# Kernel tuning notes

Measured on AMD Instinct MI355X. Metric: run time of the kernel, lower is better.

## Reference

```python
import jax, jax.numpy as jnp
import numpy as np

VOCAB, EMB, HID, L = 100000, 128, 256, 9
B, S = 128, 512
H = HID // 2  # per-direction hidden size
PAD = 0


def setup_inputs() -> dict:
    key = jax.random.key(0)
    ks = jax.random.split(key, 18)
    seqs = jax.random.randint(ks[0], (B, S), 1, VOCAB)
    # left-aligned padding: lengths in [S//2, S]
    lens = jax.random.randint(ks[1], (B,), S // 2, S + 1)
    seqs = jnp.where(jnp.arange(S)[None, :] < lens[:, None], seqs, PAD)
    labels = jax.random.randint(ks[2], (B, S), 0, L)

    def n(k, shape, s=0.05):
        return jax.random.normal(k, shape, jnp.float32) * s

    emb = n(ks[3], (VOCAB, EMB)).at[PAD].set(0.0)
    inp = {
        'sequences': seqs, 'labels': labels, 'emb': emb,
        'w_ih_f': n(ks[4], (4 * H, EMB)), 'w_hh_f': n(ks[5], (4 * H, H)),
        'b_ih_f': n(ks[6], (4 * H,)), 'b_hh_f': n(ks[7], (4 * H,)),
        'w_ih_b': n(ks[8], (4 * H, EMB)), 'w_hh_b': n(ks[9], (4 * H, H)),
        'b_ih_b': n(ks[10], (4 * H,)), 'b_hh_b': n(ks[11], (4 * H,)),
        'w_out': n(ks[12], (L, HID)), 'b_out': n(ks[13], (L,)),
        'start_t': n(ks[14], (L,), 0.1), 'end_t': n(ks[15], (L,), 0.1),
        'trans': n(ks[16], (L, L), 0.1),
    }
    return inp


def _lstm_scan(x, w_ih, w_hh, b_ih, b_hh):
    # x: [S, B, E] -> hidden states [S, B, H]
    h0 = jnp.zeros((x.shape[1], w_hh.shape[1]), x.dtype)

    def step(carry, xt):
        h, c = carry
        g = xt @ w_ih.T + b_ih + h @ w_hh.T + b_hh
        i, f, gg, o = jnp.split(g, 4, axis=-1)  # PyTorch gate order i,f,g,o
        c = jax.nn.sigmoid(f) * c + jax.nn.sigmoid(i) * jnp.tanh(gg)
        h = jax.nn.sigmoid(o) * jnp.tanh(c)
        return (h, c), h

    _, hs = jax.lax.scan(step, (h0, h0), x)
    return hs


def reference(sequences, labels, emb, w_ih_f, w_hh_f, b_ih_f, b_hh_f,
              w_ih_b, w_hh_b, b_ih_b, b_hh_b, w_out, b_out,
              start_t, end_t, trans):
    # Embedding lookup (dropout is identity at inference)
    x = emb[sequences]                      # [B,S,E]
    xt = jnp.swapaxes(x, 0, 1)              # [S,B,E]
    hf = _lstm_scan(xt, w_ih_f, w_hh_f, b_ih_f, b_hh_f)
    hb = _lstm_scan(xt[::-1], w_ih_b, w_hh_b, b_ih_b, b_hh_b)[::-1]
    hcat = jnp.concatenate([hf, hb], axis=-1)         # [S,B,HID]
    emissions = jnp.swapaxes(hcat, 0, 1) @ w_out.T + b_out  # [B,S,L]

    mask = sequences != PAD                 # [B,S], first step all True
    maskf = mask.astype(emissions.dtype)

    # --- CRF numerator (score of gold path) ---
    em_tag = jnp.take_along_axis(emissions, labels[..., None], axis=2)[..., 0]  # [B,S]
    trans_sc = trans[labels[:, :-1], labels[:, 1:]]                              # [B,S-1]
    num = start_t[labels[:, 0]] + em_tag[:, 0] \
        + jnp.sum((trans_sc + em_tag[:, 1:]) * maskf[:, 1:], axis=1)
    seq_ends = jnp.sum(mask, axis=1) - 1
    last_tags = labels[jnp.arange(labels.shape[0]), seq_ends]
    num = num + end_t[last_tags]

    # --- CRF partition function (forward algorithm) ---
    def fstep(score, inp):
        em_t, m_t = inp  # [B,L], [B]
        nxt = jax.nn.logsumexp(score[:, :, None] + trans[None] + em_t[:, None, :], axis=1)
        return jnp.where(m_t[:, None], nxt, score), None

    score0 = start_t[None, :] + emissions[:, 0]  # [B,L]
    em_rest = jnp.swapaxes(emissions, 0, 1)[1:]  # [S-1,B,L]
    scoreT, _ = jax.lax.scan(fstep, score0, (em_rest, mask.T[1:]))
    denom = jax.nn.logsumexp(scoreT + end_t[None, :], axis=1)  # [B]

    # model returns -log_likelihood (torchcrf default reduction='sum')
    return -jnp.sum(num - denom)
```

## Files before the change

### kernel.cpp

```cpp
#include <hip/hip_runtime.h>
#include <hip/hip_bf16.h>

#define B_   128
#define S_   512
#define H_   128
#define G_   512
#define EMB_ 128
#define NL_  9

typedef __attribute__((ext_vector_type(8))) short bf16x8;
typedef __attribute__((ext_vector_type(4))) short bf16x4;
typedef __attribute__((ext_vector_type(4))) float f32x4;
typedef unsigned short ushort_t;

__device__ __forceinline__ void wg_bar() {
    asm volatile("s_waitcnt lgkmcnt(0)\n\ts_barrier" ::: "memory");
}

__device__ __forceinline__ float bfbits2f(short s) {
    unsigned int u = ((unsigned int)(unsigned short)s) << 16;
    return __builtin_bit_cast(float, u);
}
__device__ __forceinline__ short f2bf(float f) {
    unsigned int u = __builtin_bit_cast(unsigned int, f);
    u += 0x7FFFu + ((u >> 16) & 1u);
    return (short)(u >> 16);
}
__device__ __forceinline__ unsigned int pack2(float lo, float hi) {
    return (unsigned int)(unsigned short)f2bf(lo) | ((unsigned int)(unsigned short)f2bf(hi) << 16);
}
__device__ __forceinline__ float exp2_(float x) {
    float r; asm("v_exp_f32 %0, %1" : "=v"(r) : "v"(x)); return r;
}
__device__ __forceinline__ float log2_(float x) {
    float r; asm("v_log_f32 %0, %1" : "=v"(r) : "v"(x)); return r;
}
__device__ __forceinline__ float max3_(float a, float b, float c) {
    float r; asm("v_max3_f32 %0, %1, %2, %3" : "=v"(r) : "v"(a), "v"(b), "v"(c)); return r;
}
__device__ __forceinline__ float tanh_(float x) {
    return 1.f - 2.f * __builtin_amdgcn_rcpf(1.f + exp2_(2.8853900817779268f * x));
}
__device__ __forceinline__ bf16x8 cvt8(float4 a, float4 b) {
    bf16x8 r;
    r[0] = f2bf(a.x); r[1] = f2bf(a.y); r[2] = f2bf(a.z); r[3] = f2bf(a.w);
    r[4] = f2bf(b.x); r[5] = f2bf(b.y); r[6] = f2bf(b.z); r[7] = f2bf(b.w);
    return r;
}

#define MINIGEMM(tl, bufsel)                                                       \
    {                                                                              \
      f32x4 x0 = {biasI[tl][0], biasI[tl][0], biasI[tl][0], biasI[tl][0]};         \
      f32x4 x1 = {biasI[tl][1], biasI[tl][1], biasI[tl][1], biasI[tl][1]};         \
      f32x4 x2 = {biasI[tl][2], biasI[tl][2], biasI[tl][2], biasI[tl][2]};         \
      f32x4 x3 = {biasI[tl][3], biasI[tl][3], biasI[tl][3], biasI[tl][3]};         \
      x0 = __builtin_amdgcn_mfma_f32_16x16x32_bf16(afE0, bfragI[tl][0][0], x0, 0, 0, 0); \
      x1 = __builtin_amdgcn_mfma_f32_16x16x32_bf16(afE0, bfragI[tl][1][0], x1, 0, 0, 0); \
      x2 = __builtin_amdgcn_mfma_f32_16x16x32_bf16(afE0, bfragI[tl][2][0], x2, 0, 0, 0); \
      x3 = __builtin_amdgcn_mfma_f32_16x16x32_bf16(afE0, bfragI[tl][3][0], x3, 0, 0, 0); \
      x0 = __builtin_amdgcn_mfma_f32_16x16x32_bf16(afE1, bfragI[tl][0][1], x0, 0, 0, 0); \
      x1 = __builtin_amdgcn_mfma_f32_16x16x32_bf16(afE1, bfragI[tl][1][1], x1, 0, 0, 0); \
      x2 = __builtin_amdgcn_mfma_f32_16x16x32_bf16(afE1, bfragI[tl][2][1], x2, 0, 0, 0); \
      x3 = __builtin_amdgcn_mfma_f32_16x16x32_bf16(afE1, bfragI[tl][3][1], x3, 0, 0, 0); \
      x0 = __builtin_amdgcn_mfma_f32_16x16x32_bf16(afE2, bfragI[tl][0][2], x0, 0, 0, 0); \
      x1 = __builtin_amdgcn_mfma_f32_16x16x32_bf16(afE2, bfragI[tl][1][2], x1, 0, 0, 0); \
      x2 = __builtin_amdgcn_mfma_f32_16x16x32_bf16(afE2, bfragI[tl][2][2], x2, 0, 0, 0); \
      x3 = __builtin_amdgcn_mfma_f32_16x16x32_bf16(afE2, bfragI[tl][3][2], x3, 0, 0, 0); \
      x0 = __builtin_amdgcn_mfma_f32_16x16x32_bf16(afE3, bfragI[tl][0][3], x0, 0, 0, 0); \
      x1 = __builtin_amdgcn_mfma_f32_16x16x32_bf16(afE3, bfragI[tl][1][3], x1, 0, 0, 0); \
      x2 = __builtin_amdgcn_mfma_f32_16x16x32_bf16(afE3, bfragI[tl][2][3], x2, 0, 0, 0); \
      x3 = __builtin_amdgcn_mfma_f32_16x16x32_bf16(afE3, bfragI[tl][3][3], x3, 0, 0, 0); \
      short* dstp = xwSW + (bufsel) * 8192 + (wv * 32 + (tl) * 16 + n16) * 4;      \
      _Pragma("unroll")                                                            \
      for (int r = 0; r < 4; r++) {                                                \
        uint2 wq; wq.x = pack2(x0[r], x1[r]); wq.y = pack2(x2[r], x3[r]);          \
        *(uint2*)(dstp + (quad * 4 + r) * 512) = wq;                               \
      }                                                                            \
    }

#define STEPK(k)                                                                   \
  {                                                                                \
    if ((k) == 0 && s4 == 0 && m < 31) {                                           \
      int t0s = dir ? (S_ - 32 - m16) : (m16 + 16);                                \
      int tok = seq[b * S_ + t0s + n16];                                           \
      const float* ep = emb + (size_t)tok * EMB_ + quad * 8;                       \
      e0 = *(const float4*)(ep);        e1 = *(const float4*)(ep + 4);             \
      e2 = *(const float4*)(ep + 32);   e3 = *(const float4*)(ep + 36);            \
      e4 = *(const float4*)(ep + 64);   e5 = *(const float4*)(ep + 68);            \
      e6 = *(const float4*)(ep + 96);   e7 = *(const float4*)(ep + 100);           \
    }                                                                              \
    bf16x8 af0 = hbuf[(k) & 1][0 * 4 + quad];                                      \
    bf16x8 af1 = hbuf[(k) & 1][1 * 4 + quad];                                      \
    bf16x8 af2 = hbuf[(k) & 1][2 * 4 + quad];                                      \
    bf16x8 af3 = hbuf[(k) & 1][3 * 4 + quad];                                      \
    const int KE = s4x4 + (k);                                                     \
    const int slot = dir ? (15 - KE) : KE;                                         \
    bf16x4 xvg = *(const bf16x4*)(xwS + (m & 1) * 8192 + slot * 512 + uu * 4);     \
    if ((k) == 0 && s4 == 1 && m < 31) { afE0 = cvt8(e0, e1); afE1 = cvt8(e2, e3); } \
    if ((k) == 2 && s4 == 1 && m < 31) { afE2 = cvt8(e4, e5); afE3 = cvt8(e6, e7); } \
    if ((k) == 0 && s4 == 2 && m < 31) MINIGEMM(0, ((m & 1) ^ 1))                  \
    if ((k) == 2 && s4 == 2 && m < 31) MINIGEMM(1, ((m & 1) ^ 1))                  \
    if ((k) == 1 && s4 == 0 && m >= 1 && wv == 3 && lane < 36) {                   \
      int a0 = dir ? (S_ - m16) : (m16 - 16);                                      \
      float4 fv = *(const float4*)(emL + (a0 & 31) * 9 + lane * 4);                \
      *(float4*)(emdir + (size_t)b * (S_ * NL_) + a0 * NL_ + lane * 4) = fv;       \
    }                                                                              \
    f32x4 aA0 = __builtin_amdgcn_mfma_f32_16x16x32_bf16(af0, bfrag[0][0][0], ZACC, 0, 0, 0); \
    f32x4 aA1 = __builtin_amdgcn_mfma_f32_16x16x32_bf16(af0, bfrag[0][1][0], ZACC, 0, 0, 0); \
    f32x4 aA2 = __builtin_amdgcn_mfma_f32_16x16x32_bf16(af0, bfrag[0][2][0], ZACC, 0, 0, 0); \
    f32x4 aA3 = __builtin_amdgcn_mfma_f32_16x16x32_bf16(af0, bfrag[0][3][0], ZACC, 0, 0, 0); \
    f32x4 aB0 = __builtin_amdgcn_mfma_f32_16x16x32_bf16(af0, bfrag[1][0][0], ZACC, 0, 0, 0); \
    f32x4 aB1 = __builtin_amdgcn_mfma_f32_16x16x32_bf16(af0, bfrag[1][1][0], ZACC, 0, 0, 0); \
    f32x4 aB2 = __builtin_amdgcn_mfma_f32_16x16x32_bf16(af0, bfrag[1][2][0], ZACC, 0, 0, 0); \
    f32x4 aB3 = __builtin_amdgcn_mfma_f32_16x16x32_bf16(af0, bfrag[1][3][0], ZACC, 0, 0, 0); \
    aA0 = __builtin_amdgcn_mfma_f32_16x16x32_bf16(af1, bfrag[0][0][1], aA0, 0, 0, 0); \
    aA1 = __builtin_amdgcn_mfma_f32_16x16x32_bf16(af1, bfrag[0][1][1], aA1, 0, 0, 0); \
    aA2 = __builtin_amdgcn_mfma_f32_16x16x32_bf16(af1, bfrag[0][2][1], aA2, 0, 0, 0); \
    aA3 = __builtin_amdgcn_mfma_f32_16x16x32_bf16(af1, bfrag[0][3][1], aA3, 0, 0, 0); \
    aB0 = __builtin_amdgcn_mfma_f32_16x16x32_bf16(af1, bfrag[1][0][1], aB0, 0, 0, 0); \
    aB1 = __builtin_amdgcn_mfma_f32_16x16x32_bf16(af1, bfrag[1][1][1], aB1, 0, 0, 0); \
    aB2 = __builtin_amdgcn_mfma_f32_16x16x32_bf16(af1, bfrag[1][2][1], aB2, 0, 0, 0); \
    aB3 = __builtin_amdgcn_mfma_f32_16x16x32_bf16(af1, bfrag[1][3][1], aB3, 0, 0, 0); \
    aA0 = __builtin_amdgcn_mfma_f32_16x16x32_bf16(af2, bfrag[0][0][2], aA0, 0, 0, 0); \
    aA1 = __builtin_amdgcn_mfma_f32_16x16x32_bf16(af2, bfrag[0][1][2], aA1, 0, 0, 0); \
    aA2 = __builtin_amdgcn_mfma_f32_16x16x32_bf16(af2, bfrag[0][2][2], aA2, 0, 0, 0); \
    aA3 = __builtin_amdgcn_mfma_f32_16x16x32_bf16(af2, bfrag[0][3][2], aA3, 0, 0, 0); \
    aB0 = __builtin_amdgcn_mfma_f32_16x16x32_bf16(af2, bfrag[1][0][2], aB0, 0, 0, 0); \
    aB1 = __builtin_amdgcn_mfma_f32_16x16x32_bf16(af2, bfrag[1][1][2], aB1, 0, 0, 0); \
    aB2 = __builtin_amdgcn_mfma_f32_16x16x32_bf16(af2, bfrag[1][2][2], aB2, 0, 0, 0); \
    aB3 = __builtin_amdgcn_mfma_f32_16x16x32_bf16(af2, bfrag[1][3][2], aB3, 0, 0, 0); \
    aA0 = __builtin_amdgcn_mfma_f32_16x16x32_bf16(af3, bfrag[0][0][3], aA0, 0, 0, 0); \
    aA1 = __builtin_amdgcn_mfma_f32_16x16x32_bf16(af3, bfrag[0][1][3], aA1, 0, 0, 0); \
    aA2 = __builtin_amdgcn_mfma_f32_16x16x32_bf16(af3, bfrag[0][2][3], aA2, 0, 0, 0); \
    aA3 = __builtin_amdgcn_mfma_f32_16x16x32_bf16(af3, bfrag[0][3][3], aA3, 0, 0, 0); \
    aB0 = __builtin_amdgcn_mfma_f32_16x16x32_bf16(af3, bfrag[1][0][3], aB0, 0, 0, 0); \
    aB1 = __builtin_amdgcn_mfma_f32_16x16x32_bf16(af3, bfrag[1][1][3], aB1, 0, 0, 0); \
    aB2 = __builtin_amdgcn_mfma_f32_16x16x32_bf16(af3, bfrag[1][2][3], aB2, 0, 0, 0); \
    aB3 = __builtin_amdgcn_mfma_f32_16x16x32_bf16(af3, bfrag[1][3][3], aB3, 0, 0, 0); \
    {                                                                              \
      float gi = ((quad & 2) ? aB0[0] : aA0[0]) + bfbits2f(xvg[0]);                \
      float gf = ((quad & 2) ? aB1[0] : aA1[0]) + bfbits2f(xvg[1]);                \
      float gg = ((quad & 2) ? aB2[0] : aA2[0]) + bfbits2f(xvg[2]);                \
      float go = ((quad & 2) ? aB3[0] : aA3[0]) + bfbits2f(xvg[3]);                \
      float Af = exp2_(-1.4426950408889634f * gf);                                 \
      float Bi = exp2_(-1.4426950408889634f * gi);                                 \
      float Cg = exp2_(2.8853900817779268f * gg);                                  \
      float Fo = exp2_(-1.4426950408889634f * go);                                 \
      float oA = 1.f + Af, oB = 1.f + Bi, oC = 1.f + Cg;                           \
      float P = oB * oC;                                                           \
      float numer = cst * P + oA * (Cg - 1.f);                                     \
      cst = numer * __builtin_amdgcn_rcpf(oA * P);                                 \
      float hv = tanh_(cst) * __builtin_amdgcn_rcpf(1.f + Fo);                     \
      if (!(quad & 1)) *(((k) & 1) ? hw0 : hw1) = f2bf(hv);                        \
    }                                                                              \
    if (wv == 0) {                                                                 \
      f32x4 accE = __builtin_amdgcn_mfma_f32_16x16x32_bf16(af0, bfragE[0], ZACC, 0, 0, 0); \
      accE = __builtin_amdgcn_mfma_f32_16x16x32_bf16(af1, bfragE[1], accE, 0, 0, 0); \
      accE = __builtin_amdgcn_mfma_f32_16x16x32_bf16(af2, bfragE[2], accE, 0, 0, 0); \
      accE = __builtin_amdgcn_mfma_f32_16x16x32_bf16(af3, bfragE[3], accE, 0, 0, 0); \
      if (quad == 0 && n16 < NL_ && (m16 + KE) >= 1) {                             \
        int tprev = dir ? (S_ - (m16 + KE)) : (m16 + KE - 1);                      \
        emL[(tprev & 31) * 9 + n16] = accE[0];                                     \
      }                                                                            \
    }                                                                              \
    wg_bar();                                                                      \
  }

__global__ __launch_bounds__(256, 1)
void lstm_kernel(const int* __restrict__ seq, const float* __restrict__ emb,
                 const float* __restrict__ w_ih_f, const float* __restrict__ b_ih_f,
                 const float* __restrict__ b_hh_f,
                 const float* __restrict__ w_ih_b, const float* __restrict__ b_ih_b,
                 const float* __restrict__ b_hh_b,
                 const float* __restrict__ w_hh_f, const float* __restrict__ w_hh_b,
                 const float* __restrict__ w_out,
                 float* __restrict__ em_f, float* __restrict__ em_b)
{
    __shared__ bf16x8 xwL[2 * 1024];
    __shared__ bf16x8 hbuf[2][16];
    __shared__ __align__(16) float emL[32 * NL_];

    const int tid  = threadIdx.x;
    const int wv   = tid >> 6;
    const int lane = tid & 63;
    const int n16  = tid & 15;
    const int quad = (tid & 63) >> 4;
    const int dir  = blockIdx.x >> 7;
    const int b    = blockIdx.x & 127;

    const int uu = wv * 32 + ((quad >> 1) << 4) + n16;

    short* hw0 = ((short*)hbuf) + uu;
    short* hw1 = ((short*)hbuf) + 128 + uu;
    const short* xwS = (const short*)xwL;
    short* xwSW = (short*)xwL;

    const f32x4 ZACC = {0.f, 0.f, 0.f, 0.f};

    const float* whh = dir ? w_hh_b : w_hh_f;
    const float* wih = dir ? w_ih_b : w_ih_f;
    const float* bih = dir ? b_ih_b : b_ih_f;
    const float* bhh = dir ? b_hh_b : b_hh_f;
    float* emdir = dir ? em_b : em_f;

    bf16x8 bfrag[2][4][4];
#pragma unroll
    for (int tl = 0; tl < 2; tl++) {
#pragma unroll
        for (int nt = 0; nt < 4; nt++) {
            int col = nt * 128 + wv * 32 + tl * 16 + n16;
#pragma unroll
            for (int ks = 0; ks < 4; ks++) {
                const float* p = whh + col * H_ + ks * 32 + quad * 8;
                bf16x8 fr;
#pragma unroll
                for (int j = 0; j < 8; j++) fr[j] = f2bf(p[j]);
                bfrag[tl][nt][ks] = fr;
            }
        }
    }
    bf16x8 bfragI[2][4][4];
    float  biasI[2][4];
#pragma unroll
    for (int tl = 0; tl < 2; tl++) {
#pragma unroll
        for (int nt = 0; nt < 4; nt++) {
            int col = nt * 128 + wv * 32 + tl * 16 + n16;
            biasI[tl][nt] = bih[col] + bhh[col];
#pragma unroll
            for (int ks = 0; ks < 4; ks++) {
                const float* p = wih + col * EMB_ + ks * 32 + quad * 8;
                bf16x8 fr;
#pragma unroll
                for (int j = 0; j < 8; j++) fr[j] = f2bf(p[j]);
                bfragI[tl][nt][ks] = fr;
            }
        }
    }
    bf16x8 bfragE[4];
#pragma unroll
    for (int ks = 0; ks < 4; ks++) {
        bf16x8 fr = {0, 0, 0, 0, 0, 0, 0, 0};
        if (n16 < NL_) {
            const float* p = w_out + n16 * 256 + dir * 128 + ks * 32 + quad * 8;
#pragma unroll
            for (int j = 0; j < 8; j++) fr[j] = f2bf(p[j]);
        }
        bfragE[ks] = fr;
    }

    if (tid < 64) ((int*)hbuf)[tid] = 0;

    float4 e0, e1, e2, e3, e4, e5, e6, e7;
    bf16x8 afE0, afE1, afE2, afE3;

    {
        int t0s = dir ? (S_ - 16) : 0;
        int tok = seq[b * S_ + t0s + n16];
        const float* ep = emb + (size_t)tok * EMB_ + quad * 8;
        e0 = *(const float4*)(ep);        e1 = *(const float4*)(ep + 4);
        e2 = *(const float4*)(ep + 32);   e3 = *(const float4*)(ep + 36);
        e4 = *(const float4*)(ep + 64);   e5 = *(const float4*)(ep + 68);
        e6 = *(const float4*)(ep + 96);   e7 = *(const float4*)(ep + 100);
        afE0 = cvt8(e0, e1); afE1 = cvt8(e2, e3);
        afE2 = cvt8(e4, e5); afE3 = cvt8(e6, e7);
        MINIGEMM(0, 0)
        MINIGEMM(1, 0)
    }

    float cst = 0.f;
    wg_bar();

#pragma unroll 1
    for (int m = 0; m < 32; m++) {
        const int m16 = m << 4;
#pragma unroll 1
        for (int s4 = 0; s4 < 4; s4++) {
            const int s4x4 = s4 << 2;
            STEPK(0) STEPK(1) STEPK(2) STEPK(3)
        }
    }

    if (wv == 0) {
        bf16x8 af0 = hbuf[0][0 * 4 + quad];
        bf16x8 af1 = hbuf[0][1 * 4 + quad];
        bf16x8 af2 = hbuf[0][2 * 4 + quad];
        bf16x8 af3 = hbuf[0][3 * 4 + quad];
        f32x4 accE = __builtin_amdgcn_mfma_f32_16x16x32_bf16(af0, bfragE[0], ZACC, 0, 0, 0);
        accE = __builtin_amdgcn_mfma_f32_16x16x32_bf16(af1, bfragE[1], accE, 0, 0, 0);
        accE = __builtin_amdgcn_mfma_f32_16x16x32_bf16(af2, bfragE[2], accE, 0, 0, 0);
        accE = __builtin_amdgcn_mfma_f32_16x16x32_bf16(af3, bfragE[3], accE, 0, 0, 0);
        if (quad == 0 && n16 < NL_) {
            int tprev = dir ? 0 : (S_ - 1);
            emL[(tprev & 31) * 9 + n16] = accE[0];
        }
    }
    wg_bar();
    if (wv == 3 && lane < 36) {
        int a0 = dir ? 0 : (S_ - 16);
        float4 fv = *(const float4*)(emL + (a0 & 31) * 9 + lane * 4);
        *(float4*)(emdir + (size_t)b * (S_ * NL_) + a0 * NL_ + lane * 4) = fv;
    }
}

__global__ __launch_bounds__(640, 1)
void crf_kernel(const int* __restrict__ seq, const int* __restrict__ lab,
                const float* __restrict__ em_f, const float* __restrict__ em_b,
                const float* __restrict__ b_out,
                const float* __restrict__ start_t, const float* __restrict__ end_t,
                const float* __restrict__ trans, float* __restrict__ partial)
{
    __shared__ float emS[S_ * NL_];
    __shared__ float transS[NL_ * NL_];
    __shared__ float stS[NL_], enS[NL_];
    __shared__ unsigned char maskS[S_];
    __shared__ float MS[7 * 81];
    __shared__ float vS[NL_];
    __shared__ float redw[10];
    __shared__ int   redl[10];

    const int b = blockIdx.x, tid = threadIdx.x;
    const size_t base = (size_t)b * S_ * NL_;
    const float L2E = 1.4426950408889634f, LN2 = 0.6931471805599453f;

    for (int q = tid; q < S_ * NL_; q += 640)
        emS[q] = em_f[base + q] + em_b[base + q] + b_out[q % NL_];
    if (tid < NL_ * NL_) transS[tid] = trans[tid];
    if (tid < NL_) { stS[tid] = start_t[tid]; enS[tid] = end_t[tid]; }
    if (tid < S_) maskS[tid] = (seq[b * S_ + tid] != 0);
    __syncthreads();

    float np = 0.f; int myc = 0;
    if (tid < S_) {
        myc = maskS[tid];
        if (tid >= 1 && maskS[tid]) {
            int lp = lab[b * S_ + tid - 1], lc = lab[b * S_ + tid];
            np = transS[lp * NL_ + lc] + emS[tid * NL_ + lc];
        }
    }
#pragma unroll
    for (int off = 32; off; off >>= 1) {
        np  += __shfl_down(np, off, 64);
        myc += __shfl_down(myc, off, 64);
    }
    if ((tid & 63) == 0) { redw[tid >> 6] = np; redl[tid >> 6] = myc; }

    const int w = tid >> 6, l = tid & 63;
    const int lg = l / 9;
    const int g  = w * 7 + lg;
    const bool sact = (lg < 7) && (g < 64);
    const int jj = sact ? (l - lg * 9) : 0;
    const int gb = sact ? lg * 9 : 0;
    float Tc[NL_];
#pragma unroll
    for (int i = 0; i < NL_; i++) Tc[i] = transS[i * NL_ + jj];
    float sc; int tbeg, tend, cN = 0, iN = 0;
    if (sact && g == 0) {
        sc = stS[jj] + emS[jj];
        tbeg = 1; tend = 64;
    } else if (sact) {
        cN = 1 + (g - 1) / 9; iN = (g - 1) % 9;
        sc = (jj == iN) ? 0.f : -1e30f;
        tbeg = cN * 64; tend = tbeg + 64;
    } else {
        sc = -1e30f; tbeg = 448; tend = 512;
    }
    for (int t = tbeg; t < tend; t++) {
        float emv = emS[t * NL_ + jj];
        float a[NL_];
#pragma unroll
        for (int i = 0; i < NL_; i++) a[i] = __shfl(sc, gb + i, 64) + Tc[i];
        float m = max3_(max3_(a[0], a[1], a[2]), max3_(a[3], a[4], a[5]),
                        max3_(a[6], a[7], a[8]));
        float e[NL_];
#pragma unroll
        for (int i = 0; i < NL_; i++) e[i] = exp2_((a[i] - m) * L2E);
        float sum = ((e[0] + e[1]) + (e[2] + e[3])) + ((e[4] + e[5]) + (e[6] + e[7])) + e[8];
        float nxt = emv + m + LN2 * log2_(sum);
        sc = maskS[t] ? nxt : sc;
    }
    if (sact) {
        if (g == 0) vS[jj] = sc;
        else MS[(cN - 1) * 81 + iN * NL_ + jj] = sc;
    }
    __syncthreads();

    if (tid < 64) {
        const int j = (tid < NL_) ? tid : (NL_ - 1);
        float v = vS[j];
        for (int c = 1; c < 8; c++) {
            float a[NL_];
#pragma unroll
            for (int i = 0; i < NL_; i++)
                a[i] = __shfl(v, i, 64) + MS[(c - 1) * 81 + i * NL_ + j];
            float m = max3_(max3_(a[0], a[1], a[2]), max3_(a[3], a[4], a[5]),
                            max3_(a[6], a[7], a[8]));
            float e[NL_];
#pragma unroll
            for (int i = 0; i < NL_; i++) e[i] = exp2_((a[i] - m) * L2E);
            float sum = ((e[0] + e[1]) + (e[2] + e[3])) + ((e[4] + e[5]) + (e[6] + e[7])) + e[8];
            v = m + LN2 * log2_(sum);
        }
        v += enS[j];
        float mm = -1e30f, av[NL_];
#pragma unroll
        for (int i = 0; i < NL_; i++) { float vi = __shfl(v, i, 64); av[i] = vi; mm = fmaxf(mm, vi); }
        float ss = 0.f;
#pragma unroll
        for (int i = 0; i < NL_; i++) ss += exp2_((av[i] - mm) * L2E);
        if (tid == 0) {
            float num = 0.f; int len = 0;
#pragma unroll
            for (int ww = 0; ww < 10; ww++) { num += redw[ww]; len += redl[ww]; }
            int l0 = lab[b * S_];
            int ll = lab[b * S_ + len - 1];
            num += stS[l0] + emS[l0] + enS[ll];
            partial[b] = (mm + LN2 * log2_(ss)) - num;
        }
    }
}

__global__ __launch_bounds__(128)
void reduce_kernel(const float* __restrict__ partial, float* __restrict__ out)
{
    __shared__ float s[128];
    int tid = threadIdx.x;
    s[tid] = partial[tid];
    __syncthreads();
    for (int off = 64; off; off >>= 1) {
        if (tid < off) s[tid] += s[tid + off];
        __syncthreads();
    }
    if (tid == 0) out[0] = s[0];
}

extern "C" void kernel_launch(void* const* d_in, const int* in_sizes, int n_in,
                              void* d_out, int out_size, void* d_ws, size_t ws_size,
                              hipStream_t stream)
{
    const int* seq = (const int*)d_in[0];
    const int* lab = (const int*)d_in[1];
    const float* emb    = (const float*)d_in[2];
    const float* w_ih_f = (const float*)d_in[3];
    const float* w_hh_f = (const float*)d_in[4];
    const float* b_ih_f = (const float*)d_in[5];
    const float* b_hh_f = (const float*)d_in[6];
    const float* w_ih_b = (const float*)d_in[7];
    const float* w_hh_b = (const float*)d_in[8];
    const float* b_ih_b = (const float*)d_in[9];
    const float* b_hh_b = (const float*)d_in[10];
    const float* w_out  = (const float*)d_in[11];
    const float* b_out  = (const float*)d_in[12];
    const float* start_t = (const float*)d_in[13];
    const float* end_t   = (const float*)d_in[14];
    const float* trans   = (const float*)d_in[15];

    char* ws = (char*)d_ws;
    const size_t em_bytes = (size_t)B_ * S_ * NL_ * sizeof(float);
    float* em_f    = (float*)ws;
    float* em_b    = (float*)(ws + em_bytes);
    float* partial = (float*)(ws + 2 * em_bytes);

    lstm_kernel<<<dim3(256), dim3(256), 0, stream>>>(seq, emb,
        w_ih_f, b_ih_f, b_hh_f, w_ih_b, b_ih_b, b_hh_b,
        w_hh_f, w_hh_b, w_out, em_f, em_b);
    crf_kernel<<<dim3(B_), dim3(640), 0, stream>>>(seq, lab, em_f, em_b, b_out,
        start_t, end_t, trans, partial);
    reduce_kernel<<<dim3(1), dim3(128), 0, stream>>>(partial, (float*)d_out);
}
```

Measured before the change: 513.9 us.

## Pre-convert embedding table and W_ih to packed bf16 in a prep kernel

Adds a prep kernel that converts the whole 100k-row embedding table to bf16, packs W_ih into MFMA fragment order and folds the two biases into one. The LSTM kernel then streams the W_ih fragments from global/L2 each step instead of holding them in registers, and spreads the input-projection MFMAs across the k sub-steps. The aim is to free registers, shorten the per-step critical path and remove in-loop float-to-bf16 conversion. In exchange it adds a full pass over the 51 MB embedding table on every call, plus per-step global loads inside the serial recurrence.

Result: faster. 492.1 us (-4.3%).

```diff
diff --git a/kernel.cpp b/kernel.cpp
--- a/kernel.cpp
+++ b/kernel.cpp
@@ -41,53 +41,87 @@
 __device__ __forceinline__ float tanh_(float x) {
     return 1.f - 2.f * __builtin_amdgcn_rcpf(1.f + exp2_(2.8853900817779268f * x));
 }
-__device__ __forceinline__ bf16x8 cvt8(float4 a, float4 b) {
-    bf16x8 r;
-    r[0] = f2bf(a.x); r[1] = f2bf(a.y); r[2] = f2bf(a.z); r[3] = f2bf(a.w);
-    r[4] = f2bf(b.x); r[5] = f2bf(b.y); r[6] = f2bf(b.z); r[7] = f2bf(b.w);
-    return r;
-}
-
-#define MINIGEMM(tl, bufsel)                                                       \
-    {                                                                              \
-      f32x4 x0 = {biasI[tl][0], biasI[tl][0], biasI[tl][0], biasI[tl][0]};         \
-      f32x4 x1 = {biasI[tl][1], biasI[tl][1], biasI[tl][1], biasI[tl][1]};         \
-      f32x4 x2 = {biasI[tl][2], biasI[tl][2], biasI[tl][2], biasI[tl][2]};         \
-      f32x4 x3 = {biasI[tl][3], biasI[tl][3], biasI[tl][3], biasI[tl][3]};         \
-      x0 = __builtin_amdgcn_mfma_f32_16x16x32_bf16(afE0, bfragI[tl][0][0], x0, 0, 0, 0); \
-      x1 = __builtin_amdgcn_mfma_f32_16x16x32_bf16(afE0, bfragI[tl][1][0], x1, 0, 0, 0); \
-      x2 = __builtin_amdgcn_mfma_f32_16x16x32_bf16(afE0, bfragI[tl][2][0], x2, 0, 0, 0); \
-      x3 = __builtin_amdgcn_mfma_f32_16x16x32_bf16(afE0, bfragI[tl][3][0], x3, 0, 0, 0); \
-      x0 = __builtin_amdgcn_mfma_f32_16x16x32_bf16(afE1, bfragI[tl][0][1], x0, 0, 0, 0); \
-      x1 = __builtin_amdgcn_mfma_f32_16x16x32_bf16(afE1, bfragI[tl][1][1], x1, 0, 0, 0); \
-      x2 = __builtin_amdgcn_mfma_f32_16x16x32_bf16(afE1, bfragI[tl][2][1], x2, 0, 0, 0); \
-      x3 = __builtin_amdgcn_mfma_f32_16x16x32_bf16(afE1, bfragI[tl][3][1], x3, 0, 0, 0); \
-      x0 = __builtin_amdgcn_mfma_f32_16x16x32_bf16(afE2, bfragI[tl][0][2], x0, 0, 0, 0); \
-      x1 = __builtin_amdgcn_mfma_f32_16x16x32_bf16(afE2, bfragI[tl][1][2], x1, 0, 0, 0); \
-      x2 = __builtin_amdgcn_mfma_f32_16x16x32_bf16(afE2, bfragI[tl][2][2], x2, 0, 0, 0); \
-      x3 = __builtin_amdgcn_mfma_f32_16x16x32_bf16(afE2, bfragI[tl][3][2], x3, 0, 0, 0); \
-      x0 = __builtin_amdgcn_mfma_f32_16x16x32_bf16(afE3, bfragI[tl][0][3], x0, 0, 0, 0); \
-      x1 = __builtin_amdgcn_mfma_f32_16x16x32_bf16(afE3, bfragI[tl][1][3], x1, 0, 0, 0); \
-      x2 = __builtin_amdgcn_mfma_f32_16x16x32_bf16(afE3, bfragI[tl][2][3], x2, 0, 0, 0); \
-      x3 = __builtin_amdgcn_mfma_f32_16x16x32_bf16(afE3, bfragI[tl][3][3], x3, 0, 0, 0); \
-      short* dstp = xwSW + (bufsel) * 8192 + (wv * 32 + (tl) * 16 + n16) * 4;      \
-      _Pragma("unroll")                                                            \
-      for (int r = 0; r < 4; r++) {                                                \
-        uint2 wq; wq.x = pack2(x0[r], x1[r]); wq.y = pack2(x2[r], x3[r]);          \
-        *(uint2*)(dstp + (quad * 4 + r) * 512) = wq;                               \
-      }                                                                            \
-    }
+
+#define NB_EMB 6250
+#define NB_WIH 64
+__global__ __launch_bounds__(256)
+void prep_kernel(const float* __restrict__ emb,
+                 const float* __restrict__ w_ih_f, const float* __restrict__ w_ih_b,
+                 const float* __restrict__ b_ih_f, const float* __restrict__ b_hh_f,
+                 const float* __restrict__ b_ih_b, const float* __restrict__ b_hh_b,
+                 ushort_t* __restrict__ embB, ushort_t* __restrict__ wihPack,
+                 float* __restrict__ biasPack)
+{
+    const int bid = blockIdx.x, tid = threadIdx.x;
+    if (bid < NB_EMB) {
+        int base = (bid * 256 + tid) * 8;
+        float4 a = *(const float4*)(emb + base);
+        float4 c = *(const float4*)(emb + base + 4);
+        bf16x8 r;
+        r[0] = f2bf(a.x); r[1] = f2bf(a.y); r[2] = f2bf(a.z); r[3] = f2bf(a.w);
+        r[4] = f2bf(c.x); r[5] = f2bf(c.y); r[6] = f2bf(c.z); r[7] = f2bf(c.w);
+        *(bf16x8*)(embB + base) = r;
+    } else if (bid < NB_EMB + NB_WIH) {
+        int f = (bid - NB_EMB) * 256 + tid;
+        int lane = f & 63;
+        int nt = (f >> 6) & 3;
+        int ks = (f >> 8) & 3;
+        int tl = (f >> 10) & 1;
+        int wv = (f >> 11) & 3;
+        int dirq = (f >> 13) & 1;
+        int n16 = lane & 15, quad = lane >> 4;
+        const float* w = dirq ? w_ih_b : w_ih_f;
+        int col = nt * 128 + wv * 32 + tl * 16 + n16;
+        const float* p = w + col * EMB_ + ks * 32 + quad * 8;
+        bf16x8 r;
+#pragma unroll
+        for (int j = 0; j < 8; j++) r[j] = f2bf(p[j]);
+        *(bf16x8*)(wihPack + f * 8) = r;
+    } else {
+        int idx = (bid - NB_EMB - NB_WIH) * 256 + tid;
+        if (idx < 1024) {
+            int nt = idx & 3;
+            int n16 = (idx >> 2) & 15;
+            int tl = (idx >> 6) & 1;
+            int wv = (idx >> 7) & 3;
+            int dirq = (idx >> 9) & 1;
+            const float* bi = dirq ? b_ih_b : b_ih_f;
+            const float* bh = dirq ? b_hh_b : b_hh_f;
+            int col = nt * 128 + wv * 32 + tl * 16 + n16;
+            biasPack[idx] = bi[col] + bh[col];
+        }
+    }
+}
+
+#define AFE_(k) afE##k
 
 #define STEPK(k)                                                                   \
   {                                                                                \
     if ((k) == 0 && s4 == 0 && m < 31) {                                           \
       int t0s = dir ? (S_ - 32 - m16) : (m16 + 16);                                \
       int tok = seq[b * S_ + t0s + n16];                                           \
-      const float* ep = emb + (size_t)tok * EMB_ + quad * 8;                       \
-      e0 = *(const float4*)(ep);        e1 = *(const float4*)(ep + 4);             \
-      e2 = *(const float4*)(ep + 32);   e3 = *(const float4*)(ep + 36);            \
-      e4 = *(const float4*)(ep + 64);   e5 = *(const float4*)(ep + 68);            \
-      e6 = *(const float4*)(ep + 96);   e7 = *(const float4*)(ep + 100);           \
+      const ushort_t* ep = embB + (size_t)tok * EMB_ + quad * 8;                   \
+      afE0 = *(const bf16x8*)(ep);                                                 \
+      afE1 = *(const bf16x8*)(ep + 32);                                            \
+      afE2 = *(const bf16x8*)(ep + 64);                                            \
+      afE3 = *(const bf16x8*)(ep + 96);                                            \
+    }                                                                              \
+    bf16x8 fr0, fr1, fr2, fr3;                                                     \
+    int tlr = 0;                                                                   \
+    if (s4 >= 2 && m < 31) {                                                       \
+      tlr = s4 - 2;                                                                \
+      const ushort_t* wp = wvbase + (tlr * 4 + (k)) * 2048;                        \
+      fr0 = *(const bf16x8*)(wp);                                                  \
+      fr1 = *(const bf16x8*)(wp + 512);                                            \
+      fr2 = *(const bf16x8*)(wp + 1024);                                           \
+      fr3 = *(const bf16x8*)(wp + 1536);                                           \
+      if ((k) == 0) {                                                              \
+        float4 bv = tlr ? bb1 : bb0;                                               \
+        x0 = (f32x4){bv.x, bv.x, bv.x, bv.x};                                      \
+        x1 = (f32x4){bv.y, bv.y, bv.y, bv.y};                                      \
+        x2 = (f32x4){bv.z, bv.z, bv.z, bv.z};                                      \
+        x3 = (f32x4){bv.w, bv.w, bv.w, bv.w};                                      \
+      }                                                                            \
     }                                                                              \
     bf16x8 af0 = hbuf[(k) & 1][0 * 4 + quad];                                      \
     bf16x8 af1 = hbuf[(k) & 1][1 * 4 + quad];                                      \
@@ -96,10 +130,6 @@
     const int KE = s4x4 + (k);                                                     \
     const int slot = dir ? (15 - KE) : KE;                                         \
     bf16x4 xvg = *(const bf16x4*)(xwS + (m & 1) * 8192 + slot * 512 + uu * 4);     \
-    if ((k) == 0 && s4 == 1 && m < 31) { afE0 = cvt8(e0, e1); afE1 = cvt8(e2, e3); } \
-    if ((k) == 2 && s4 == 1 && m < 31) { afE2 = cvt8(e4, e5); afE3 = cvt8(e6, e7); } \
-    if ((k) == 0 && s4 == 2 && m < 31) MINIGEMM(0, ((m & 1) ^ 1))                  \
-    if ((k) == 2 && s4 == 2 && m < 31) MINIGEMM(1, ((m & 1) ^ 1))                  \
     if ((k) == 1 && s4 == 0 && m >= 1 && wv == 3 && lane < 36) {                   \
       int a0 = dir ? (S_ - m16) : (m16 - 16);                                      \
       float4 fv = *(const float4*)(emL + (a0 & 31) * 9 + lane * 4);                \
@@ -137,6 +167,20 @@
     aB1 = __builtin_amdgcn_mfma_f32_16x16x32_bf16(af3, bfrag[1][1][3], aB1, 0, 0, 0); \
     aB2 = __builtin_amdgcn_mfma_f32_16x16x32_bf16(af3, bfrag[1][2][3], aB2, 0, 0, 0); \
     aB3 = __builtin_amdgcn_mfma_f32_16x16x32_bf16(af3, bfrag[1][3][3], aB3, 0, 0, 0); \
+    if (s4 >= 2 && m < 31) {                                                       \
+      x0 = __builtin_amdgcn_mfma_f32_16x16x32_bf16(AFE_(k), fr0, x0, 0, 0, 0);     \
+      x1 = __builtin_amdgcn_mfma_f32_16x16x32_bf16(AFE_(k), fr1, x1, 0, 0, 0);     \
+      x2 = __builtin_amdgcn_mfma_f32_16x16x32_bf16(AFE_(k), fr2, x2, 0, 0, 0);     \
+      x3 = __builtin_amdgcn_mfma_f32_16x16x32_bf16(AFE_(k), fr3, x3, 0, 0, 0);     \
+      if ((k) == 3) {                                                              \
+        short* dstp = xwSW + (((m & 1) ^ 1) * 8192) + (wv * 32 + tlr * 16 + n16) * 4; \
+        _Pragma("unroll")                                                          \
+        for (int r = 0; r < 4; r++) {                                              \
+          uint2 wq; wq.x = pack2(x0[r], x1[r]); wq.y = pack2(x2[r], x3[r]);        \
+          *(uint2*)(dstp + (quad * 4 + r) * 512) = wq;                             \
+        }                                                                          \
+      }                                                                            \
+    }                                                                              \
     {                                                                              \
       float gi = ((quad & 2) ? aB0[0] : aA0[0]) + bfbits2f(xvg[0]);                \
       float gf = ((quad & 2) ? aB1[0] : aA1[0]) + bfbits2f(xvg[1]);                \
@@ -167,11 +211,8 @@
   }
 
 __global__ __launch_bounds__(256, 1)
-void lstm_kernel(const int* __restrict__ seq, const float* __restrict__ emb,
-                 const float* __restrict__ w_ih_f, const float* __restrict__ b_ih_f,
-                 const float* __restrict__ b_hh_f,
-                 const float* __restrict__ w_ih_b, const float* __restrict__ b_ih_b,
-                 const float* __restrict__ b_hh_b,
+void lstm_kernel(const int* __restrict__ seq, const ushort_t* __restrict__ embB,
+                 const ushort_t* __restrict__ wihPack, const float* __restrict__ biasPack,
                  const float* __restrict__ w_hh_f, const float* __restrict__ w_hh_b,
                  const float* __restrict__ w_out,
                  float* __restrict__ em_f, float* __restrict__ em_b)
@@ -198,9 +239,6 @@
     const f32x4 ZACC = {0.f, 0.f, 0.f, 0.f};
 
     const float* whh = dir ? w_hh_b : w_hh_f;
-    const float* wih = dir ? w_ih_b : w_ih_f;
-    const float* bih = dir ? b_ih_b : b_ih_f;
-    const float* bhh = dir ? b_hh_b : b_hh_f;
     float* emdir = dir ? em_b : em_f;
 
     bf16x8 bfrag[2][4][4];
@@ -216,24 +254,6 @@
 #pragma unroll
                 for (int j = 0; j < 8; j++) fr[j] = f2bf(p[j]);
                 bfrag[tl][nt][ks] = fr;
-            }
-        }
-    }
-    bf16x8 bfragI[2][4][4];
-    float  biasI[2][4];
-#pragma unroll
-    for (int tl = 0; tl < 2; tl++) {
-#pragma unroll
-        for (int nt = 0; nt < 4; nt++) {
-            int col = nt * 128 + wv * 32 + tl * 16 + n16;
-            biasI[tl][nt] = bih[col] + bhh[col];
-#pragma unroll
-            for (int ks = 0; ks < 4; ks++) {
-                const float* p = wih + col * EMB_ + ks * 32 + quad * 8;
-                bf16x8 fr;
-#pragma unroll
-                for (int j = 0; j < 8; j++) fr[j] = f2bf(p[j]);
-                bfragI[tl][nt][ks] = fr;
             }
         }
     }
@@ -249,23 +269,50 @@
         bfragE[ks] = fr;
     }
 
+    float4 bb0 = *(const float4*)(biasPack + ((dir * 4 + wv) * 2 + 0) * 64 + n16 * 4);
+    float4 bb1 = *(const float4*)(biasPack + ((dir * 4 + wv) * 2 + 1) * 64 + n16 * 4);
+    const ushort_t* wvbase = wihPack + (size_t)(dir * 4 + wv) * 16384 + (size_t)lane * 8;
+
     if (tid < 64) ((int*)hbuf)[tid] = 0;
 
-    float4 e0, e1, e2, e3, e4, e5, e6, e7;
+    f32x4 x0, x1, x2, x3;
     bf16x8 afE0, afE1, afE2, afE3;
 
     {
         int t0s = dir ? (S_ - 16) : 0;
         int tok = seq[b * S_ + t0s + n16];
-        const float* ep = emb + (size_t)tok * EMB_ + quad * 8;
-        e0 = *(const float4*)(ep);        e1 = *(const float4*)(ep + 4);
-        e2 = *(const float4*)(ep + 32);   e3 = *(const float4*)(ep + 36);
-        e4 = *(const float4*)(ep + 64);   e5 = *(const float4*)(ep + 68);
-        e6 = *(const float4*)(ep + 96);   e7 = *(const float4*)(ep + 100);
-        afE0 = cvt8(e0, e1); afE1 = cvt8(e2, e3);
-        afE2 = cvt8(e4, e5); afE3 = cvt8(e6, e7);
-        MINIGEMM(0, 0)
-        MINIGEMM(1, 0)
+        const ushort_t* ep = embB + (size_t)tok * EMB_ + quad * 8;
+        afE0 = *(const bf16x8*)(ep);
+        afE1 = *(const bf16x8*)(ep + 32);
+        afE2 = *(const bf16x8*)(ep + 64);
+        afE3 = *(const bf16x8*)(ep + 96);
+#pragma unroll
+        for (int tl = 0; tl < 2; tl++) {
+            float4 bv = tl ? bb1 : bb0;
+            x0 = (f32x4){bv.x, bv.x, bv.x, bv.x};
+            x1 = (f32x4){bv.y, bv.y, bv.y, bv.y};
+            x2 = (f32x4){bv.z, bv.z, bv.z, bv.z};
+            x3 = (f32x4){bv.w, bv.w, bv.w, bv.w};
+#pragma unroll
+            for (int ks = 0; ks < 4; ks++) {
+                const ushort_t* wp = wvbase + (tl * 4 + ks) * 2048;
+                bf16x8 f0 = *(const bf16x8*)(wp);
+                bf16x8 f1 = *(const bf16x8*)(wp + 512);
+                bf16x8 f2 = *(const bf16x8*)(wp + 1024);
+                bf16x8 f3 = *(const bf16x8*)(wp + 1536);
+                bf16x8 ae = (ks == 0) ? afE0 : (ks == 1) ? afE1 : (ks == 2) ? afE2 : afE3;
+                x0 = __builtin_amdgcn_mfma_f32_16x16x32_bf16(ae, f0, x0, 0, 0, 0);
+                x1 = __builtin_amdgcn_mfma_f32_16x16x32_bf16(ae, f1, x1, 0, 0, 0);
+                x2 = __builtin_amdgcn_mfma_f32_16x16x32_bf16(ae, f2, x2, 0, 0, 0);
+                x3 = __builtin_amdgcn_mfma_f32_16x16x32_bf16(ae, f3, x3, 0, 0, 0);
+            }
+            short* dstp = xwSW + (wv * 32 + tl * 16 + n16) * 4;
+#pragma unroll
+            for (int r = 0; r < 4; r++) {
+                uint2 wq; wq.x = pack2(x0[r], x1[r]); wq.y = pack2(x2[r], x3[r]);
+                *(uint2*)(dstp + (quad * 4 + r) * 512) = wq;
+            }
+        }
     }
 
     float cst = 0.f;
@@ -456,13 +503,21 @@
     const float* trans   = (const float*)d_in[15];
 
     char* ws = (char*)d_ws;
-    const size_t em_bytes = (size_t)B_ * S_ * NL_ * sizeof(float);
-    float* em_f    = (float*)ws;
-    float* em_b    = (float*)(ws + em_bytes);
-    float* partial = (float*)(ws + 2 * em_bytes);
-
-    lstm_kernel<<<dim3(256), dim3(256), 0, stream>>>(seq, emb,
-        w_ih_f, b_ih_f, b_hh_f, w_ih_b, b_ih_b, b_hh_b,
+    const size_t embB_bytes = (size_t)100000 * EMB_ * sizeof(ushort_t);
+    const size_t wih_bytes  = (size_t)16384 * 16;
+    const size_t bias_bytes = 1024 * sizeof(float);
+    const size_t em_bytes   = (size_t)B_ * S_ * NL_ * sizeof(float);
+
+    ushort_t* embB    = (ushort_t*)ws;
+    ushort_t* wihPack = (ushort_t*)(ws + embB_bytes);
+    float* biasPack   = (float*)(ws + embB_bytes + wih_bytes);
+    float* em_f       = (float*)(ws + embB_bytes + wih_bytes + bias_bytes);
+    float* em_b       = (float*)(ws + embB_bytes + wih_bytes + bias_bytes + em_bytes);
+    float* partial    = (float*)(ws + embB_bytes + wih_bytes + bias_bytes + 2 * em_bytes);
+
+    prep_kernel<<<dim3(NB_EMB + NB_WIH + 4), dim3(256), 0, stream>>>(emb,
+        w_ih_f, w_ih_b, b_ih_f, b_hh_f, b_ih_b, b_hh_b, embB, wihPack, biasPack);
+    lstm_kernel<<<dim3(256), dim3(256), 0, stream>>>(seq, embB, wihPack, biasPack,
         w_hh_f, w_hh_b, w_out, em_f, em_b);
     crf_kernel<<<dim3(B_), dim3(640), 0, stream>>>(seq, lab, em_f, em_b, b_out,
         start_t, end_t, trans, partial);
```
